# Kernel optimization log

Hardware: AMD Instinct MI355X
Metric: run time of the kernel (lower is better)

Reference implementation:

```python
import jax, jax.numpy as jnp
import numpy as np

GAMMA = 0.9865


def setup_inputs() -> dict:
    key = jax.random.key(0)
    ks = jax.random.split(key, 6)
    B, T, DIN, D = 8, 2048, 1024, 1024
    return {
        "xq": jax.random.normal(ks[0], (B, T, DIN), dtype=jnp.float32),
        "xk": jax.random.normal(ks[1], (B, T, DIN), dtype=jnp.float32),
        "xv": jax.random.normal(ks[2], (B, T, DIN), dtype=jnp.float32),
        "Wq": jax.random.normal(ks[3], (DIN, D), dtype=jnp.float32) * (DIN ** -0.5),
        "Wk": jax.random.normal(ks[4], (DIN, D), dtype=jnp.float32) * (DIN ** -0.5),
        "Wv": jax.random.normal(ks[5], (DIN, D), dtype=jnp.float32) * (DIN ** -0.5),
    }


def reference(xq, xk, xv, Wq, Wk, Wv):
    # Dense projections (no bias)
    Q = jnp.einsum("btd,de->bte", xq, Wq)  # [B,T,D]
    K = jnp.einsum("btd,de->bte", xk, Wk)
    V = jnp.einsum("btd,de->bte", xv, Wv)

    # einsum('ib,bj->bj', K_t^T, V_t) == (sum_i K[b,t,i]) * V[b,t,:]
    ksum = jnp.sum(K, axis=-1)            # [B,T]
    u = ksum[..., None] * V               # [B,T,D]
    # recurrence starts at t=1 with s[0]=0, so u[0] never contributes
    u = u * (jnp.arange(u.shape[1]) > 0)[None, :, None]

    def step(s, u_t):
        s = s * jnp.float32(GAMMA) + u_t
        return s, s

    s0 = jnp.zeros(u.shape[::2], dtype=u.dtype)          # [B,D]
    _, S = jax.lax.scan(step, s0, jnp.swapaxes(u, 0, 1))  # S: [T,B,D]
    return Q * jnp.swapaxes(S, 0, 1)                      # [B,T,D]
```

## Files before the change

### kernel.cpp

```cpp
#include <hip/hip_runtime.h>
#include <hip/hip_bf16.h>

#define GAMMA 0.9865f

typedef __attribute__((ext_vector_type(8))) short bf16x8;
typedef __attribute__((ext_vector_type(4))) float f32x4;

static constexpr int Bb  = 8;
static constexpr int Tt  = 2048;
static constexpr int DIN = 1024;
static constexpr int Dd  = 1024;
static constexpr int Mm  = Bb * Tt;
static constexpr int CL  = 64;
static constexpr int NC  = Tt / CL;
static constexpr int NT  = DIN / 64;

__device__ __forceinline__ void gload16(const void* g, void* l) {
  __builtin_amdgcn_global_load_lds(
      (const __attribute__((address_space(1))) void*)g,
      (__attribute__((address_space(3))) void*)l, 16, 0, 0);
}

__device__ __forceinline__ void bar() {
  asm volatile("" ::: "memory");
  __builtin_amdgcn_s_barrier();
  asm volatile("" ::: "memory");
}

__global__ void wsum_kernel(const float* __restrict__ Wk, float* __restrict__ wsum) {
  int row  = blockIdx.x * 4 + (threadIdx.x >> 6);
  int lane = threadIdx.x & 63;
  const float4* rp = (const float4*)(Wk + (size_t)row * DIN);
  float s = 0.f;
#pragma unroll
  for (int i = 0; i < 4; ++i) {
    float4 v = rp[lane + i * 64];
    s += v.x + v.y + v.z + v.w;
  }
  for (int off = 32; off; off >>= 1) s += __shfl_down(s, off);
  if (lane == 0) wsum[row] = s;
}

__global__ void wt_kernel(const float* __restrict__ Wq, const float* __restrict__ Wv,
                          __hip_bfloat16* __restrict__ Wt) {
  const float* W = blockIdx.z ? Wv : Wq;
  __hip_bfloat16* outp = Wt + (size_t)blockIdx.z * DIN * Dd;
  __shared__ float tile[32][33];
  int k0 = blockIdx.x * 32, n0 = blockIdx.y * 32;
  int tx = threadIdx.x, ty = threadIdx.y;
#pragma unroll
  for (int i = 0; i < 4; ++i)
    tile[ty + i * 8][tx] = W[(size_t)(k0 + ty + i * 8) * Dd + n0 + tx];
  __syncthreads();
#pragma unroll
  for (int i = 0; i < 4; ++i)
    outp[(size_t)(n0 + ty + i * 8) * DIN + k0 + tx] =
        __float2bfloat16(tile[tx][ty + i * 8]);
}

__global__ void cast_kernel(const float* __restrict__ xq, const float* __restrict__ xv,
                            __hip_bfloat16* __restrict__ oq, __hip_bfloat16* __restrict__ ov) {
  const float* src = blockIdx.y ? xv : xq;
  __hip_bfloat16* dst = blockIdx.y ? ov : oq;
  size_t i = (size_t)blockIdx.x * 256 + threadIdx.x;
  float4 v = ((const float4*)src)[i];
  union { __hip_bfloat16 h[4]; ushort4 u; } cv;
  cv.h[0] = __float2bfloat16(v.x);
  cv.h[1] = __float2bfloat16(v.y);
  cv.h[2] = __float2bfloat16(v.z);
  cv.h[3] = __float2bfloat16(v.w);
  ((ushort4*)dst)[i] = cv.u;
}


__device__ __forceinline__ void stage_half(const __hip_bfloat16* g, char* l, int tid) {
#pragma unroll
  for (int j = 0; j < 2; ++j) {
    int c = tid + j * 512;
    int row = c >> 3, ch = c & 7;
    gload16(g + (size_t)row * DIN + ((ch ^ (row & 7)) << 3), l + c * 16);
  }
}

__device__ __forceinline__ bf16x8 lds_frag(const char* base, int row, int kc) {
  return *(const bf16x8*)(base + (((row << 3) + (kc ^ (row & 7))) << 4));
}

#define MFMA_QUAD(MLO, NLO)                                                  \
  _Pragma("unroll") for (int mi = 0; mi < 4; ++mi)                           \
  _Pragma("unroll") for (int ni = 0; ni < 2; ++ni)                           \
  _Pragma("unroll") for (int ks = 0; ks < 2; ++ks)                           \
      acc[(MLO) + mi][(NLO) + ni] = __builtin_amdgcn_mfma_f32_16x16x32_bf16( \
          a[(MLO) + mi][ks], b[(NLO) + ni][ks], acc[(MLO) + mi][(NLO) + ni], 0, 0, 0);

__global__ __launch_bounds__(512, 2) void gemm8_kernel(
    const __hip_bfloat16* __restrict__ Aq, const __hip_bfloat16* __restrict__ Av,
    const __hip_bfloat16* __restrict__ Wt,
    __hip_bfloat16* __restrict__ Qbf, __hip_bfloat16* __restrict__ Vbf) {
  extern __shared__ char lds[];

  int lin = blockIdx.x;
  int wg  = (lin & 7) * 64 + (lin >> 3);
  int z   = wg >> 8, rem = wg & 255;
  int by  = rem & 3, bx = rem >> 2;

  const __hip_bfloat16* Ab = z ? Av : Aq;
  const int m0 = bx * 256, n0 = by * 256;
  const __hip_bfloat16* Ag = Ab + (size_t)m0 * DIN;
  const __hip_bfloat16* Bg = Wt + ((size_t)z * Dd + n0) * DIN;
  __hip_bfloat16* Cc = z ? Vbf : Qbf;

  const int tid = threadIdx.x;
  const int wv = tid >> 6, lane = tid & 63;
  const int wm = (wv >> 2) * 128, wn = (wv & 3) * 64;
  const int fq = lane >> 4, fr = lane & 15;

  f32x4 acc[8][4] = {};

  stage_half(Ag,                  lds,                 tid);
  stage_half(Ag + 128 * DIN,      lds + 16384,         tid);
  stage_half(Bg,                  lds + 32768,         tid);
  stage_half(Bg + 128 * DIN,      lds + 49152,         tid);
  stage_half(Ag + 64,             lds + 65536,         tid);
  stage_half(Ag + 128 * DIN + 64, lds + 65536 + 16384, tid);
  asm volatile("s_waitcnt vmcnt(4)" ::: "memory");
  bar();

  for (int t = 0; t < NT; ++t) {
    char* buf  = lds + (t & 1) * 65536;
    char* bufN = lds + ((t + 1) & 1) * 65536;
    const char* At = buf;
    const char* Bt = buf + 32768;
    bf16x8 a[8][2], b[4][2];

#pragma unroll
    for (int mi = 0; mi < 4; ++mi)
#pragma unroll
      for (int ks = 0; ks < 2; ++ks)
        a[mi][ks] = lds_frag(At, wm + mi * 16 + fr, ks * 4 + fq);
#pragma unroll
    for (int ni = 0; ni < 2; ++ni)
#pragma unroll
      for (int ks = 0; ks < 2; ++ks)
        b[ni][ks] = lds_frag(Bt, wn + ni * 16 + fr, ks * 4 + fq);
    if (t + 1 < NT) stage_half(Bg + (size_t)(t + 1) * 64, bufN + 32768, tid);
    bar();
    __builtin_amdgcn_s_setprio(1);
    MFMA_QUAD(0, 0);
    __builtin_amdgcn_s_setprio(0);
    bar();

#pragma unroll
    for (int mi = 4; mi < 8; ++mi)
#pragma unroll
      for (int ks = 0; ks < 2; ++ks)
        a[mi][ks] = lds_frag(At, wm + mi * 16 + fr, ks * 4 + fq);
    if (t + 1 < NT)
      stage_half(Bg + 128 * DIN + (size_t)(t + 1) * 64, bufN + 49152, tid);
    bar();
    __builtin_amdgcn_s_setprio(1);
    MFMA_QUAD(4, 0);
    __builtin_amdgcn_s_setprio(0);
    bar();

#pragma unroll
    for (int ni = 2; ni < 4; ++ni)
#pragma unroll
      for (int ks = 0; ks < 2; ++ks)
        b[ni][ks] = lds_frag(Bt, wn + ni * 16 + fr, ks * 4 + fq);
    if (t + 2 < NT) stage_half(Ag + (size_t)(t + 2) * 64, buf, tid);
    bar();
    __builtin_amdgcn_s_setprio(1);
    MFMA_QUAD(0, 2);
    __builtin_amdgcn_s_setprio(0);
    bar();

    if (t + 2 < NT)
      stage_half(Ag + 128 * DIN + (size_t)(t + 2) * 64, buf + 16384, tid);
    if (t + 1 < NT) {
      if (t + 2 < NT) asm volatile("s_waitcnt vmcnt(4)" ::: "memory");
      else            asm volatile("s_waitcnt vmcnt(0)" ::: "memory");
    }
    bar();
    __builtin_amdgcn_s_setprio(1);
    MFMA_QUAD(4, 2);
    __builtin_amdgcn_s_setprio(0);
    bar();
  }

#pragma unroll
  for (int mi = 0; mi < 8; ++mi) {
#pragma unroll
    for (int ni = 0; ni < 4; ++ni) {
      f32x4 v = acc[mi][ni];
      int row = m0 + wm + mi * 16 + fq * 4;
      int col = n0 + wn + ni * 16 + fr;
#pragma unroll
      for (int j = 0; j < 4; ++j)
        Cc[(size_t)(row + j) * Dd + col] = __float2bfloat16(v[j]);
    }
  }
}

__global__ void ksum_kernel(const float* __restrict__ xk, const float* __restrict__ wsum,
                            float* __restrict__ ksum) {
  int row  = blockIdx.x * 4 + (threadIdx.x >> 6);
  int lane = threadIdx.x & 63;
  const float4* rp = (const float4*)(xk + (size_t)row * DIN);
  const float4* wp = (const float4*)wsum;
  float s = 0.f;
#pragma unroll
  for (int i = 0; i < 4; ++i) {
    float4 a = rp[lane + i * 64];
    float4 w = wp[lane + i * 64];
    s += a.x * w.x + a.y * w.y + a.z * w.z + a.w * w.w;
  }
  for (int off = 32; off; off >>= 1) s += __shfl_down(s, off);
  if (lane == 0) ksum[row] = s;
}

__global__ void scanA_kernel(const __hip_bfloat16* __restrict__ Vbf,
                             const float* __restrict__ ksum,
                             float* __restrict__ E) {
  int b = blockIdx.x, c = blockIdx.y;
  int d = blockIdx.z * 256 + threadIdx.x;
  const __hip_bfloat16* Vp = Vbf + ((size_t)(b * Tt + c * CL) * Dd) + d;
  const float* kp = ksum + b * Tt + c * CL;
  float s = 0.f;
#pragma unroll 8
  for (int t = 0; t < CL; ++t) {
    float u = kp[t] * __bfloat162float(Vp[(size_t)t * Dd]);
    if (c == 0 && t == 0) u = 0.f;
    s = s * GAMMA + u;
  }
  E[((size_t)b * NC + c) * Dd + d] = s;
}

__global__ void scanB_kernel(const float* __restrict__ E, float* __restrict__ carry,
                             float gCL) {
  int b = blockIdx.x;
  int d = blockIdx.y * 256 + threadIdx.x;
  float send = 0.f;
  for (int c = 0; c < NC; ++c) {
    size_t idx = ((size_t)b * NC + c) * Dd + d;
    float e = E[idx];
    carry[idx] = send;
    send = e + gCL * send;
  }
}

__global__ void final_kernel(const __hip_bfloat16* __restrict__ Vbf,
                             const __hip_bfloat16* __restrict__ Qbf,
                             const float* __restrict__ ksum,
                             const float* __restrict__ carry,
                             float* __restrict__ outp) {
  int b = blockIdx.x, c = blockIdx.y;
  int d = blockIdx.z * 256 + threadIdx.x;
  size_t base = ((size_t)(b * Tt + c * CL) * Dd) + d;
  float s = carry[((size_t)b * NC + c) * Dd + d];
  const float* kp = ksum + b * Tt + c * CL;
#pragma unroll 4
  for (int t = 0; t < CL; ++t) {
    float u = kp[t] * __bfloat162float(Vbf[base + (size_t)t * Dd]);
    if (c == 0 && t == 0) u = 0.f;
    s = s * GAMMA + u;
    outp[base + (size_t)t * Dd] = __bfloat162float(Qbf[base + (size_t)t * Dd]) * s;
  }
}

extern "C" void kernel_launch(void* const* d_in, const int* in_sizes, int n_in,
                              void* d_out, int out_size, void* d_ws, size_t ws_size,
                              hipStream_t stream) {
  (void)in_sizes; (void)n_in; (void)out_size; (void)ws_size;
  const float* xq = (const float*)d_in[0];
  const float* xk = (const float*)d_in[1];
  const float* xv = (const float*)d_in[2];
  const float* Wq = (const float*)d_in[3];
  const float* Wk = (const float*)d_in[4];
  const float* Wv = (const float*)d_in[5];
  float* outp = (float*)d_out;

  char* ws = (char*)d_ws;
  size_t off = 0;
  auto alloc = [&](size_t bytes) {
    char* p = ws + off;
    off += (bytes + 255) & ~(size_t)255;
    return p;
  };
  __hip_bfloat16* xq_bf = (__hip_bfloat16*)alloc((size_t)Mm * DIN * 2);
  __hip_bfloat16* xv_bf = (__hip_bfloat16*)alloc((size_t)Mm * DIN * 2);
  __hip_bfloat16* Wt    = (__hip_bfloat16*)alloc((size_t)2 * DIN * Dd * 2);
  __hip_bfloat16* Qbf   = (__hip_bfloat16*)alloc((size_t)Mm * Dd * 2);
  __hip_bfloat16* Vbf   = (__hip_bfloat16*)alloc((size_t)Mm * Dd * 2);
  float* wsum  = (float*)alloc((size_t)DIN * 4);
  float* ksum  = (float*)alloc((size_t)Mm * 4);
  float* E     = (float*)alloc((size_t)Bb * NC * Dd * 4);
  float* carry = (float*)alloc((size_t)Bb * NC * Dd * 4);

  double g = 1.0;
  for (int i = 0; i < CL; ++i) g *= (double)GAMMA;
  float gCL = (float)g;

  (void)hipFuncSetAttribute((const void*)gemm8_kernel,
                            hipFuncAttributeMaxDynamicSharedMemorySize, 131072);

  wsum_kernel<<<DIN / 4, 256, 0, stream>>>(Wk, wsum);
  wt_kernel<<<dim3(DIN / 32, Dd / 32, 2), dim3(32, 8), 0, stream>>>(Wq, Wv, Wt);
  cast_kernel<<<dim3(Mm * DIN / 4 / 256, 2), 256, 0, stream>>>(xq, xv, xq_bf, xv_bf);
  gemm8_kernel<<<512, 512, 131072, stream>>>(xq_bf, xv_bf, Wt, Qbf, Vbf);
  ksum_kernel<<<Mm / 4, 256, 0, stream>>>(xk, wsum, ksum);
  scanA_kernel<<<dim3(Bb, NC, Dd / 256), 256, 0, stream>>>(Vbf, ksum, E);
  scanB_kernel<<<dim3(Bb, Dd / 256), 256, 0, stream>>>(E, carry, gCL);
  final_kernel<<<dim3(Bb, NC, Dd / 256), 256, 0, stream>>>(Vbf, Qbf, ksum, carry, outp);
}
```

Baseline: 158.2 us.

## Fuse fp32-to-bf16 activation cast into GEMM A-tile staging

```diff
diff --git a/kernel.cpp b/kernel.cpp
--- a/kernel.cpp
+++ b/kernel.cpp
@@ -58,20 +58,6 @@
         __float2bfloat16(tile[tx][ty + i * 8]);
 }
 
-__global__ void cast_kernel(const float* __restrict__ xq, const float* __restrict__ xv,
-                            __hip_bfloat16* __restrict__ oq, __hip_bfloat16* __restrict__ ov) {
-  const float* src = blockIdx.y ? xv : xq;
-  __hip_bfloat16* dst = blockIdx.y ? ov : oq;
-  size_t i = (size_t)blockIdx.x * 256 + threadIdx.x;
-  float4 v = ((const float4*)src)[i];
-  union { __hip_bfloat16 h[4]; ushort4 u; } cv;
-  cv.h[0] = __float2bfloat16(v.x);
-  cv.h[1] = __float2bfloat16(v.y);
-  cv.h[2] = __float2bfloat16(v.z);
-  cv.h[3] = __float2bfloat16(v.w);
-  ((ushort4*)dst)[i] = cv.u;
-}
-
 
 __device__ __forceinline__ void stage_half(const __hip_bfloat16* g, char* l, int tid) {
 #pragma unroll
@@ -79,6 +65,30 @@
     int c = tid + j * 512;
     int row = c >> 3, ch = c & 7;
     gload16(g + (size_t)row * DIN + ((ch ^ (row & 7)) << 3), l + c * 16);
+  }
+}
+
+__device__ __forceinline__ void loadA2(const float* Ag, int t, int tid, int h, float4* f) {
+#pragma unroll
+  for (int j = 0; j < 2; ++j) {
+    int c = tid + (h * 2 + j) * 512;
+    int row = c >> 3, ch = c & 7;
+    const float4* p = (const float4*)(Ag + (size_t)row * DIN + t * 64 + ch * 8);
+    f[(h * 2 + j) * 2 + 0] = p[0];
+    f[(h * 2 + j) * 2 + 1] = p[1];
+  }
+}
+
+__device__ __forceinline__ void writeA(char* bufA, int tid, const float4* f) {
+#pragma unroll
+  for (int j = 0; j < 4; ++j) {
+    int c = tid + j * 512;
+    int row = c >> 3, ch = c & 7;
+    union { __hip_bfloat16 h[8]; bf16x8 v; } u;
+    const float* fp = (const float*)(f + j * 2);
+#pragma unroll
+    for (int i = 0; i < 8; ++i) u.h[i] = __float2bfloat16(fp[i]);
+    *(bf16x8*)(bufA + (((row << 3) + (ch ^ (row & 7))) << 4)) = u.v;
   }
 }
 
@@ -94,7 +104,7 @@
           a[(MLO) + mi][ks], b[(NLO) + ni][ks], acc[(MLO) + mi][(NLO) + ni], 0, 0, 0);
 
 __global__ __launch_bounds__(512, 2) void gemm8_kernel(
-    const __hip_bfloat16* __restrict__ Aq, const __hip_bfloat16* __restrict__ Av,
+    const float* __restrict__ Aq, const float* __restrict__ Av,
     const __hip_bfloat16* __restrict__ Wt,
     __hip_bfloat16* __restrict__ Qbf, __hip_bfloat16* __restrict__ Vbf) {
   extern __shared__ char lds[];
@@ -104,9 +114,9 @@
   int z   = wg >> 8, rem = wg & 255;
   int by  = rem & 3, bx = rem >> 2;
 
-  const __hip_bfloat16* Ab = z ? Av : Aq;
+  const float* Ab = z ? Av : Aq;
   const int m0 = bx * 256, n0 = by * 256;
-  const __hip_bfloat16* Ag = Ab + (size_t)m0 * DIN;
+  const float* Ag = Ab + (size_t)m0 * DIN;
   const __hip_bfloat16* Bg = Wt + ((size_t)z * Dd + n0) * DIN;
   __hip_bfloat16* Cc = z ? Vbf : Qbf;
 
@@ -117,14 +127,17 @@
 
   f32x4 acc[8][4] = {};
 
-  stage_half(Ag,                  lds,                 tid);
-  stage_half(Ag + 128 * DIN,      lds + 16384,         tid);
-  stage_half(Bg,                  lds + 32768,         tid);
-  stage_half(Bg + 128 * DIN,      lds + 49152,         tid);
-  stage_half(Ag + 64,             lds + 65536,         tid);
-  stage_half(Ag + 128 * DIN + 64, lds + 65536 + 16384, tid);
-  asm volatile("s_waitcnt vmcnt(4)" ::: "memory");
-  bar();
+  {
+    stage_half(Bg,             lds + 32768, tid);
+    stage_half(Bg + 128 * DIN, lds + 49152, tid);
+    float4 f[8];
+    loadA2(Ag, 0, tid, 0, f); loadA2(Ag, 0, tid, 1, f);
+    writeA(lds, tid, f);
+    loadA2(Ag, 1, tid, 0, f); loadA2(Ag, 1, tid, 1, f);
+    writeA(lds + 65536, tid, f);
+    asm volatile("s_waitcnt vmcnt(0) lgkmcnt(0)" ::: "memory");
+    bar();
+  }
 
   for (int t = 0; t < NT; ++t) {
     char* buf  = lds + (t & 1) * 65536;
@@ -132,6 +145,7 @@
     const char* At = buf;
     const char* Bt = buf + 32768;
     bf16x8 a[8][2], b[4][2];
+    float4 fA[8];
 
 #pragma unroll
     for (int mi = 0; mi < 4; ++mi)
@@ -151,36 +165,34 @@
     bar();
 
 #pragma unroll
+    for (int ni = 2; ni < 4; ++ni)
+#pragma unroll
+      for (int ks = 0; ks < 2; ++ks)
+        b[ni][ks] = lds_frag(Bt, wn + ni * 16 + fr, ks * 4 + fq);
+    if (t + 1 < NT)
+      stage_half(Bg + 128 * DIN + (size_t)(t + 1) * 64, bufN + 49152, tid);
+    if (t + 2 < NT) loadA2(Ag, t + 2, tid, 0, fA);
+    bar();
+    __builtin_amdgcn_s_setprio(1);
+    MFMA_QUAD(0, 2);
+    __builtin_amdgcn_s_setprio(0);
+    bar();
+
+#pragma unroll
     for (int mi = 4; mi < 8; ++mi)
 #pragma unroll
       for (int ks = 0; ks < 2; ++ks)
         a[mi][ks] = lds_frag(At, wm + mi * 16 + fr, ks * 4 + fq);
-    if (t + 1 < NT)
-      stage_half(Bg + 128 * DIN + (size_t)(t + 1) * 64, bufN + 49152, tid);
+    if (t + 2 < NT) loadA2(Ag, t + 2, tid, 1, fA);
     bar();
     __builtin_amdgcn_s_setprio(1);
     MFMA_QUAD(4, 0);
     __builtin_amdgcn_s_setprio(0);
     bar();
 
-#pragma unroll
-    for (int ni = 2; ni < 4; ++ni)
-#pragma unroll
-      for (int ks = 0; ks < 2; ++ks)
-        b[ni][ks] = lds_frag(Bt, wn + ni * 16 + fr, ks * 4 + fq);
-    if (t + 2 < NT) stage_half(Ag + (size_t)(t + 2) * 64, buf, tid);
-    bar();
-    __builtin_amdgcn_s_setprio(1);
-    MFMA_QUAD(0, 2);
-    __builtin_amdgcn_s_setprio(0);
-    bar();
-
-    if (t + 2 < NT)
-      stage_half(Ag + 128 * DIN + (size_t)(t + 2) * 64, buf + 16384, tid);
-    if (t + 1 < NT) {
-      if (t + 2 < NT) asm volatile("s_waitcnt vmcnt(4)" ::: "memory");
-      else            asm volatile("s_waitcnt vmcnt(0)" ::: "memory");
-    }
+    if (t + 2 < NT) writeA(buf, tid, fA);
+    if (t + 2 < NT)      asm volatile("s_waitcnt vmcnt(0) lgkmcnt(0)" ::: "memory");
+    else if (t + 1 < NT) asm volatile("s_waitcnt vmcnt(0)" ::: "memory");
     bar();
     __builtin_amdgcn_s_setprio(1);
     MFMA_QUAD(4, 2);
@@ -287,8 +299,6 @@
     off += (bytes + 255) & ~(size_t)255;
     return p;
   };
-  __hip_bfloat16* xq_bf = (__hip_bfloat16*)alloc((size_t)Mm * DIN * 2);
-  __hip_bfloat16* xv_bf = (__hip_bfloat16*)alloc((size_t)Mm * DIN * 2);
   __hip_bfloat16* Wt    = (__hip_bfloat16*)alloc((size_t)2 * DIN * Dd * 2);
   __hip_bfloat16* Qbf   = (__hip_bfloat16*)alloc((size_t)Mm * Dd * 2);
   __hip_bfloat16* Vbf   = (__hip_bfloat16*)alloc((size_t)Mm * Dd * 2);
@@ -306,8 +316,7 @@
 
   wsum_kernel<<<DIN / 4, 256, 0, stream>>>(Wk, wsum);
   wt_kernel<<<dim3(DIN / 32, Dd / 32, 2), dim3(32, 8), 0, stream>>>(Wq, Wv, Wt);
-  cast_kernel<<<dim3(Mm * DIN / 4 / 256, 2), 256, 0, stream>>>(xq, xv, xq_bf, xv_bf);
-  gemm8_kernel<<<512, 512, 131072, stream>>>(xq_bf, xv_bf, Wt, Qbf, Vbf);
+  gemm8_kernel<<<512, 512, 131072, stream>>>(xq, xv, Wt, Qbf, Vbf);
   ksum_kernel<<<Mm / 4, 256, 0, stream>>>(xk, wsum, ksum);
   scanA_kernel<<<dim3(Bb, NC, Dd / 256), 256, 0, stream>>>(Vbf, ksum, E);
   scanB_kernel<<<dim3(Bb, Dd / 256), 256, 0, stream>>>(E, carry, gCL);
```

Result: slower. 187.4 us (+18.5%).
